# Performance work log

Measured on AMD Instinct MI355X. Metric: run time of the kernel, lower is better.

The kernel has to match this reference:

```python
import jax, jax.numpy as jnp
import numpy as np


def conv1x1(x, w, b):
    # x: [B,C,H,W], w: [O,C], b: [O]
    return jnp.einsum('bchw,oc->bohw', x, w) + b[None, :, None, None]


def dwconv(x, w):
    # depthwise conv, x: [B,C,H,W], w: [C,1,k,k], SAME padding (k odd, pad=k//2)
    return jax.lax.conv_general_dilated(
        x, w, window_strides=(1, 1), padding='SAME',
        dimension_numbers=('NCHW', 'OIHW', 'NCHW'),
        feature_group_count=x.shape[1])


def setup_inputs() -> dict:
    key = jax.random.key(0)
    ks = jax.random.split(key, 14)
    B, C, H, W = 16, 256, 64, 64
    OC = C // 16  # scale=16 -> 16
    WSCALE = 0.05
    r = lambda k, shape: jax.random.normal(k, shape, dtype=jnp.float32) * WSCALE
    return {
        'x': jax.random.normal(ks[0], (B, C, H, W), dtype=jnp.float32),
        'conv_w': r(ks[1], (C + 4, C)),           # 1x1 conv -> ctx (C) + gates (3+1)
        'conv_b': r(ks[2], (C + 4,)),
        'fw3': r(ks[3], (C, 1, 3, 3)),            # depthwise focal kernels
        'fw5': r(ks[4], (C, 1, 5, 5)),
        'fw7': r(ks[5], (C, 1, 7, 7)),
        'key_w': r(ks[6], (1, C)),                # Conv_key 1x1
        'key_b': r(ks[7], (1,)),
        'v1_w': r(ks[8], (OC, C)),                # Conv_value first 1x1
        'v1_b': r(ks[9], (OC,)),
        'ln_w': jnp.ones((OC,), dtype=jnp.float32),
        'ln_b': jnp.zeros((OC,), dtype=jnp.float32),
        'v2_w': r(ks[10], (C, OC)),               # Conv_value second 1x1
        'v2_b': r(ks[11], (C,)),
    }


def reference(x, conv_w, conv_b, fw3, fw5, fw7, key_w, key_b,
              v1_w, v1_b, ln_w, ln_b, v2_w, v2_b):
    B, C, H, W = x.shape
    # _contextAggregation
    t = conv1x1(x, conv_w, conv_b)          # [B, C+4, H, W]
    ctx, gates = t[:, :C], t[:, C:]         # [B,C,H,W], [B,4,H,W]
    ctx_all = jnp.zeros_like(ctx)
    for l, fw in enumerate((fw3, fw5, fw7)):
        ctx = jax.nn.gelu(dwconv(ctx, fw), approximate=False)  # torch GELU = exact erf
        ctx_all = ctx_all + ctx * gates[:, l:l + 1]
    ctx_global = jnp.mean(ctx, axis=(2, 3), keepdims=True)     # AdaptiveAvgPool2d(1)
    ctx_all = ctx_all + ctx_global * gates[:, 3:4]
    # GC-style channel attention: softmax over spatial positions
    k = conv1x1(ctx_all, key_w, key_b).reshape(B, H * W)       # [B, HW]
    k = jax.nn.softmax(k, axis=1)
    q = ctx_all.reshape(B, C, H * W)
    qk = jnp.einsum('bcn,bn->bc', q, k)[:, :, None, None]      # [B,C,1,1]
    # Conv_value: 1x1 -> LayerNorm([OC,1,1]) -> ReLU -> 1x1
    v = conv1x1(qk, v1_w, v1_b)                                # [B,OC,1,1]
    mu = jnp.mean(v, axis=(1, 2, 3), keepdims=True)
    var = jnp.var(v, axis=(1, 2, 3), keepdims=True)
    v = (v - mu) * jax.lax.rsqrt(var + 1e-5)
    v = v * ln_w[None, :, None, None] + ln_b[None, :, None, None]
    v = jax.nn.relu(v)
    v = conv1x1(v, v2_w, v2_b)                                 # [B,C,1,1]
    return ctx_all + v
```

## Files before the change

kernel.cpp:

```cpp
#include <hip/hip_runtime.h>

#define DEVFN __device__ __forceinline__

constexpr int B  = 16;
constexpr int C  = 256;
constexpr int N  = 64 * 64;
constexpr int O1 = C + 4;

typedef __attribute__((ext_vector_type(8)))  short bf16x8;
typedef __attribute__((ext_vector_type(4)))  short bf16x4;
typedef __attribute__((ext_vector_type(16))) float f32x16;
typedef __attribute__((ext_vector_type(2)))  _Float16 h2;
typedef unsigned short ushort_t;
typedef unsigned int   uint32;

DEVFN short f2bf(float f){
  union { float f; unsigned u; } p; p.f = f;
  unsigned r = p.u + 0x7fffu + ((p.u >> 16) & 1u);
  return (short)(r >> 16);
}
DEVFN unsigned pack2(float lo, float hi){
  return (unsigned)(ushort_t)f2bf(lo) | ((unsigned)(ushort_t)f2bf(hi) << 16);
}
DEVFN float lo2f(unsigned u){ union{unsigned u; float f;} p; p.u = u << 16; return p.f; }
DEVFN float hi2f(unsigned u){ union{unsigned u; float f;} p; p.u = u & 0xffff0000u; return p.f; }
DEVFN float bf2f(ushort_t s){ union{unsigned u; float f;} p; p.u = (unsigned)s << 16; return p.f; }

DEVFN float gelu_fast(float x){
  float s = x * x;
  float t = x * fmaf(s, 0.1029432f, 2.3022082f);
  float e = __builtin_amdgcn_exp2f(-t);
  return x * __builtin_amdgcn_rcpf(1.0f + e);
}

DEVFN float fdot2f(uint32 a, uint32 b, float c){
#if __has_builtin(__builtin_amdgcn_fdot2)
  return __builtin_amdgcn_fdot2(__builtin_bit_cast(h2, a),
                                __builtin_bit_cast(h2, b), c, false);
#else
  h2 ha = __builtin_bit_cast(h2, a), hb = __builtin_bit_cast(h2, b);
  return fmaf((float)ha.x, (float)hb.x, fmaf((float)ha.y, (float)hb.y, c));
#endif
}

DEVFN uint32 pkh(float a, float b){
  _Float16 ha = (_Float16)a, hb = (_Float16)b;
  return (uint32)__builtin_bit_cast(ushort_t, ha) |
         ((uint32)__builtin_bit_cast(ushort_t, hb) << 16);
}

__global__ __launch_bounds__(256)
void k_wbf(const float* __restrict__ w, ushort_t* __restrict__ wbf,
           const float* __restrict__ fw3, const float* __restrict__ fw5,
           const float* __restrict__ fw7, uint32* __restrict__ w3p,
           uint32* __restrict__ w5p, uint32* __restrict__ w7p,
           const float* __restrict__ x, ushort_t* __restrict__ xbf){
  if(blockIdx.x >= 321){
    const int blk = blockIdx.x - 321;
    const int b  = blk >> 5;
    const int kg = blk & 31;
    const float* xs = x + ((size_t)(b * 256 + kg * 8)) * N;
    ushort_t* xd = xbf + ((size_t)(b * 32 + kg)) * N * 8;
    #pragma unroll
    for(int it = 0; it < 4; it++){
      const int n = (it * 256 + threadIdx.x) * 4;
      float4 cv[8];
      #pragma unroll
      for(int j = 0; j < 8; j++) cv[j] = *(const float4*)(xs + (size_t)j * N + n);
      #pragma unroll
      for(int p = 0; p < 4; p++){
        uint4 v;
        v.x = pack2(((const float*)&cv[0])[p], ((const float*)&cv[1])[p]);
        v.y = pack2(((const float*)&cv[2])[p], ((const float*)&cv[3])[p]);
        v.z = pack2(((const float*)&cv[4])[p], ((const float*)&cv[5])[p]);
        v.w = pack2(((const float*)&cv[6])[p], ((const float*)&cv[7])[p]);
        *(uint4*)(xd + (size_t)(n + p) * 8) = v;
      }
    }
    return;
  }
  if(blockIdx.x == 320){
    const int c = threadIdx.x;
    #pragma unroll
    for(int ky = 0; ky < 3; ky++){
      const float* wr = fw3 + c * 9 + ky * 3;
      w3p[c * 6 + ky * 2 + 0] = pkh(wr[0], wr[1]);
      w3p[c * 6 + ky * 2 + 1] = pkh(wr[2], 0.f);
    }
    #pragma unroll
    for(int ky = 0; ky < 5; ky++){
      const float* wr = fw5 + c * 25 + ky * 5;
      w5p[c * 15 + ky * 3 + 0] = pkh(wr[0], wr[1]);
      w5p[c * 15 + ky * 3 + 1] = pkh(wr[2], wr[3]);
      w5p[c * 15 + ky * 3 + 2] = pkh(wr[4], 0.f);
    }
    #pragma unroll
    for(int ky = 0; ky < 7; ky++){
      const float* wr = fw7 + c * 49 + ky * 7;
      w7p[c * 28 + ky * 4 + 0] = pkh(wr[0], wr[1]);
      w7p[c * 28 + ky * 4 + 1] = pkh(wr[2], wr[3]);
      w7p[c * 28 + ky * 4 + 2] = pkh(wr[4], wr[5]);
      w7p[c * 28 + ky * 4 + 3] = pkh(wr[6], 0.f);
    }
    return;
  }
  int idx = blockIdx.x * 256 + threadIdx.x;
  int o = idx >> 8, cc = idx & 255;
  wbf[idx] = (o < O1) ? (ushort_t)f2bf(w[o * 256 + cc]) : (ushort_t)0;
}

__global__ __launch_bounds__(512, 6)
void k_conv1_mfma(const ushort_t* __restrict__ xbf, const ushort_t* __restrict__ wbf,
                  const float* __restrict__ conv_w, const float* __restrict__ bias,
                  ushort_t* __restrict__ ctxb, float* __restrict__ gates){
  __shared__ __align__(16) short wlds[2][4 * 256 * 8];
  __shared__ __align__(16) short xlds[2][4 * 64 * 8];
  __shared__ float sgw[4 * 256];
  __shared__ float sbias[256];
  const int tid  = threadIdx.x;
  const int wave = tid >> 6;
  const int lane = tid & 63;
  const int l31  = lane & 31;
  const int lhi  = lane >> 5;
  const int pg   = blockIdx.x;
  const int b    = pg >> 6;
  const int n0   = (pg & 63) * 64;

  #pragma unroll
  for(int i = 0; i < 2; i++) sgw[i * 512 + tid] = conv_w[256 * 256 + i * 512 + tid];
  if(tid < 256) sbias[tid] = bias[tid];
  const int gidx = tid >> 6;
  const int gn   = tid & 63;
  float gbias = (tid < 256) ? bias[256 + gidx] : 0.f;
  float gacc = 0.f;

  f32x16 acc[2];
  #pragma unroll
  for(int t = 0; t < 2; t++)
    #pragma unroll
    for(int r = 0; r < 16; r++) acc[t][r] = 0.f;

  auto glX = [&](int kc, int bf){
    if(tid < 256){
      const int kg = tid >> 6, n = tid & 63;
      const ushort_t* src = xbf + ((size_t)(b * 32 + (kc >> 3) + kg) * N + n0 + n) * 8;
      __builtin_amdgcn_global_load_lds(
          (const __attribute__((address_space(1))) unsigned int*)src,
          (__attribute__((address_space(3))) unsigned int*)&xlds[bf][(size_t)tid * 8],
          16, 0, 0);
    }
  };
  auto glW = [&](int kc, int bf){
    #pragma unroll
    for(int q = 0; q < 2; q++){
      const int pidx = q * 512 + tid;
      const int kg = pidx >> 8;
      const int m  = pidx & 255;
      const ushort_t* src = wbf + (size_t)m * 256 + kc + kg * 8;
      __builtin_amdgcn_global_load_lds(
          (const __attribute__((address_space(1))) unsigned int*)src,
          (__attribute__((address_space(3))) unsigned int*)&wlds[bf][(size_t)pidx * 8],
          16, 0, 0);
    }
  };
  auto mfmaC = [&](int bf){
    #pragma unroll
    for(int ks = 0; ks < 2; ks++){
      const int kg = ks * 2 + lhi;
      bf16x8 af = *(const bf16x8*)&wlds[bf][(kg * 256 + wave * 32 + l31) * 8];
      bf16x8 b0 = *(const bf16x8*)&xlds[bf][(kg * 64 + l31) * 8];
      bf16x8 b1 = *(const bf16x8*)&xlds[bf][(kg * 64 + 32 + l31) * 8];
      acc[0] = __builtin_amdgcn_mfma_f32_32x32x16_bf16(af, b0, acc[0], 0, 0, 0);
      acc[1] = __builtin_amdgcn_mfma_f32_32x32x16_bf16(af, b1, acc[1], 0, 0, 0);
    }
  };
  auto gateC = [&](int bf, int kc){
    if(tid < 256){
      float a = gacc;
      #pragma unroll
      for(int kg = 0; kg < 4; kg++){
        bf16x8 xv = *(const bf16x8*)&xlds[bf][(kg * 64 + gn) * 8];
        const float* gw = &sgw[gidx * 256 + kc + kg * 8];
        #pragma unroll
        for(int j = 0; j < 4; j++){
          unsigned u = ((const unsigned*)&xv)[j];
          a = fmaf(lo2f(u), gw[2 * j], a);
          a = fmaf(hi2f(u), gw[2 * j + 1], a);
        }
      }
      gacc = a;
    }
  };

  glX(0, 0); glW(0, 0);
  __syncthreads();
  #pragma unroll
  for(int c = 0; c < 7; c++){
    const int bf = c & 1;
    glX((c + 1) * 32, bf ^ 1);
    glW((c + 1) * 32, bf ^ 1);
    mfmaC(bf);
    gateC(bf, c * 32);
    __syncthreads();
  }
  mfmaC(1);
  gateC(1, 224);

  #pragma unroll
  for(int nt = 0; nt < 2; nt++){
    const int n = n0 + nt * 32 + l31;
    #pragma unroll
    for(int r = 0; r < 16; r++){
      const int row = (r & 3) + 8 * (r >> 2) + 4 * lhi;
      const int o = wave * 32 + row;
      const float v = acc[nt][r] + sbias[o];
      _Float16 hv = (_Float16)v;
      ctxb[((size_t)(b * 256 + o)) * N + n] = __builtin_bit_cast(ushort_t, hv);
    }
  }
  if(tid < 256)
    gates[((size_t)(b * 4 + gidx)) * N + n0 + gn] = gacc + gbias;
}

constexpr int SSTR = 72;

template<int K>
DEVFN void dw_stage_dot(const short* src, const uint32* __restrict__ wp,
                        int h, int w0, float* val){
  constexpr int R = K / 2;
  constexpr int PAIRS = (K + 2) / 2;
  float acc[8];
  #pragma unroll
  for(int i = 0; i < 8; i++) acc[i] = 0.f;
  #pragma unroll
  for(int ky = 0; ky < K; ky++){
    uint32 wk[PAIRS];
    #pragma unroll
    for(int t = 0; t < PAIRS; t++) wk[t] = wp[ky * PAIRS + t];
    const int r = h + ky - R;
    if((unsigned)r < 64u){
      const short* rp = &src[r * SSTR + w0];
      uint4 a0 = *(const uint4*)rp;
      uint4 a1 = *(const uint4*)(rp + 8);
      uint32 P[8] = {a0.x, a0.y, a0.z, a0.w, a1.x, a1.y, a1.z, a1.w};
      uint32 S[7];
      #pragma unroll
      for(int j = 0; j < 7; j++)
        S[j] = __builtin_amdgcn_alignbit(P[j + 1], P[j], 16);
      #pragma unroll
      for(int i = 0; i < 8; i++){
        int j0, useP;
        if      (K == 7){ useP =  (i & 1); j0 = (i + 1) >> 1; }
        else if (K == 5){ useP = !(i & 1); j0 = (i >> 1) + 1; }
        else            { useP =  (i & 1); j0 = (i >> 1) + ((i & 1) ? 2 : 1); }
        #pragma unroll
        for(int t = 0; t < PAIRS; t++){
          const uint32 a = useP ? P[j0 + t] : S[j0 + t];
          acc[i] = fdot2f(a, wk[t], acc[i]);
        }
      }
    }
  }
  #pragma unroll
  for(int i = 0; i < 8; i++) val[i] = gelu_fast(acc[i]);
}

DEVFN void store_row_h(short* dst, int h, int w0, const float* val){
  uint32 o0 = __builtin_bit_cast(uint32, __builtin_amdgcn_cvt_pkrtz(val[0], val[1]));
  uint32 o1 = __builtin_bit_cast(uint32, __builtin_amdgcn_cvt_pkrtz(val[2], val[3]));
  uint32 o2 = __builtin_bit_cast(uint32, __builtin_amdgcn_cvt_pkrtz(val[4], val[5]));
  uint32 o3 = __builtin_bit_cast(uint32, __builtin_amdgcn_cvt_pkrtz(val[6], val[7]));
  uint2 t0; t0.x = o0; t0.y = o1;
  uint2 t1; t1.x = o2; t1.y = o3;
  *(uint2*)&dst[h * SSTR + w0 + 4] = t0;
  *(uint2*)&dst[h * SSTR + w0 + 8] = t1;
}

__global__ __launch_bounds__(512, 8)
void k_dwchain(ushort_t* __restrict__ ctxb, const uint32* __restrict__ w3p,
               const uint32* __restrict__ w5p, const uint32* __restrict__ w7p,
               const float* __restrict__ gates){
  __shared__ __align__(16) short bufA[64 * SSTR];
  __shared__ __align__(16) short bufB[64 * SSTR];
  __shared__ float wred[8];
  const int tid = threadIdx.x;
  const int plane = blockIdx.x;
  const int b = plane >> 8;
  const int c = plane & 255;
  const int h  = tid >> 3;
  const int w0 = (tid & 7) * 8;
  const int nbase = h * 64 + w0;

  if(tid < 64){
    bf16x4 z = {0, 0, 0, 0};
    *(bf16x4*)&bufA[tid * SSTR] = z;  *(bf16x4*)&bufA[tid * SSTR + 68] = z;
    *(bf16x4*)&bufB[tid * SSTR] = z;  *(bf16x4*)&bufB[tid * SSTR + 68] = z;
  }
  {
    const uint4 iv = *(const uint4*)((const short*)ctxb + (size_t)plane * N + tid * 8);
    uint2 t0; t0.x = iv.x; t0.y = iv.y;
    uint2 t1; t1.x = iv.z; t1.y = iv.w;
    *(uint2*)&bufA[h * SSTR + w0 + 4] = t0;
    *(uint2*)&bufA[h * SSTR + w0 + 8] = t1;
  }
  __syncthreads();

  float ctxp[8];
  #pragma unroll
  for(int i = 0; i < 8; i++) ctxp[i] = 0.f;
  float val[8];

  dw_stage_dot<3>(bufA, w3p + c * 6, h, w0, val);
  {
    const float* gp = gates + ((size_t)(b * 4 + 0)) * N + nbase;
    float4 ga = *(const float4*)gp, gb = *(const float4*)(gp + 4);
    ctxp[0] = fmaf(val[0], ga.x, ctxp[0]); ctxp[1] = fmaf(val[1], ga.y, ctxp[1]);
    ctxp[2] = fmaf(val[2], ga.z, ctxp[2]); ctxp[3] = fmaf(val[3], ga.w, ctxp[3]);
    ctxp[4] = fmaf(val[4], gb.x, ctxp[4]); ctxp[5] = fmaf(val[5], gb.y, ctxp[5]);
    ctxp[6] = fmaf(val[6], gb.z, ctxp[6]); ctxp[7] = fmaf(val[7], gb.w, ctxp[7]);
    store_row_h(bufB, h, w0, val);
  }
  __syncthreads();

  dw_stage_dot<5>(bufB, w5p + c * 15, h, w0, val);
  {
    const float* gp = gates + ((size_t)(b * 4 + 1)) * N + nbase;
    float4 ga = *(const float4*)gp, gb = *(const float4*)(gp + 4);
    ctxp[0] = fmaf(val[0], ga.x, ctxp[0]); ctxp[1] = fmaf(val[1], ga.y, ctxp[1]);
    ctxp[2] = fmaf(val[2], ga.z, ctxp[2]); ctxp[3] = fmaf(val[3], ga.w, ctxp[3]);
    ctxp[4] = fmaf(val[4], gb.x, ctxp[4]); ctxp[5] = fmaf(val[5], gb.y, ctxp[5]);
    ctxp[6] = fmaf(val[6], gb.z, ctxp[6]); ctxp[7] = fmaf(val[7], gb.w, ctxp[7]);
    store_row_h(bufA, h, w0, val);
  }
  __syncthreads();

  dw_stage_dot<7>(bufA, w7p + c * 28, h, w0, val);
  float lsum = 0.f;
  {
    const float* gp = gates + ((size_t)(b * 4 + 2)) * N + nbase;
    float4 ga = *(const float4*)gp, gb = *(const float4*)(gp + 4);
    ctxp[0] = fmaf(val[0], ga.x, ctxp[0]); ctxp[1] = fmaf(val[1], ga.y, ctxp[1]);
    ctxp[2] = fmaf(val[2], ga.z, ctxp[2]); ctxp[3] = fmaf(val[3], ga.w, ctxp[3]);
    ctxp[4] = fmaf(val[4], gb.x, ctxp[4]); ctxp[5] = fmaf(val[5], gb.y, ctxp[5]);
    ctxp[6] = fmaf(val[6], gb.z, ctxp[6]); ctxp[7] = fmaf(val[7], gb.w, ctxp[7]);
    #pragma unroll
    for(int i = 0; i < 8; i++) lsum += val[i];
  }
  #pragma unroll
  for(int off = 32; off > 0; off >>= 1) lsum += __shfl_xor(lsum, off, 64);
  if((tid & 63) == 0) wred[tid >> 6] = lsum;
  __syncthreads();
  float mean = 0.f;
  #pragma unroll
  for(int i = 0; i < 8; i++) mean += wred[i];
  mean *= (1.0f / 4096.0f);

  {
    const float* gp = gates + ((size_t)(b * 4 + 3)) * N + nbase;
    float4 ga = *(const float4*)gp, gb = *(const float4*)(gp + 4);
    bf16x8 ov;
    ov[0] = f2bf(fmaf(mean, ga.x, ctxp[0])); ov[1] = f2bf(fmaf(mean, ga.y, ctxp[1]));
    ov[2] = f2bf(fmaf(mean, ga.z, ctxp[2])); ov[3] = f2bf(fmaf(mean, ga.w, ctxp[3]));
    ov[4] = f2bf(fmaf(mean, gb.x, ctxp[4])); ov[5] = f2bf(fmaf(mean, gb.y, ctxp[5]));
    ov[6] = f2bf(fmaf(mean, gb.z, ctxp[6])); ov[7] = f2bf(fmaf(mean, gb.w, ctxp[7]));
    *(bf16x8*)((short*)ctxb + (size_t)plane * N + nbase) = ov;
  }
}

__global__ __launch_bounds__(256)
void k_logits(const ushort_t* __restrict__ P, const float* __restrict__ key_w,
              const float* __restrict__ key_b, float* __restrict__ logits){
  __shared__ float kw[256];
  __shared__ float part[512];
  int tid = threadIdx.x;
  kw[tid] = key_w[tid];
  __syncthreads();
  int b  = blockIdx.x >> 5;
  int n0 = (blockIdx.x & 31) * 128;
  int cpart = tid >> 6, pxp = tid & 63;
  const ushort_t* pp = P + ((size_t)(b * 256 + cpart * 64)) * N + n0 + pxp * 2;
  float a0 = 0.f, a1 = 0.f;
  #pragma unroll 8
  for(int c = 0; c < 64; c++){
    unsigned u = *(const unsigned*)(pp + (size_t)c * N);
    float kwv = kw[cpart * 64 + c];
    a0 = fmaf(lo2f(u), kwv, a0);
    a1 = fmaf(hi2f(u), kwv, a1);
  }
  part[cpart * 128 + pxp * 2]     = a0;
  part[cpart * 128 + pxp * 2 + 1] = a1;
  __syncthreads();
  if(tid < 128){
    float l = part[tid] + part[128 + tid] + part[256 + tid] + part[384 + tid];
    logits[b * N + n0 + tid] = l + key_b[0];
  }
}

__global__ __launch_bounds__(256)
void k_qk(const ushort_t* __restrict__ P, const float* __restrict__ logits,
          float* __restrict__ qk){
  __shared__ float red[256];
  __shared__ float wred[4];
  const int plane = blockIdx.x, tid = threadIdx.x;
  const int b = plane >> 8;
  const int wave = tid >> 6, lane = tid & 63;
  const float2* lp = (const float2*)(logits + b * N);
  float2 l2[8];
  float m = -1e30f;
  #pragma unroll
  for(int i = 0; i < 8; i++){
    l2[i] = lp[tid + i * 256];
    m = fmaxf(m, fmaxf(l2[i].x, l2[i].y));
  }
  #pragma unroll
  for(int off = 32; off > 0; off >>= 1) m = fmaxf(m, __shfl_xor(m, off, 64));
  if(lane == 0) wred[wave] = m;
  __syncthreads();
  m = fmaxf(fmaxf(wred[0], wred[1]), fmaxf(wred[2], wred[3]));
  __syncthreads();
  float s = 0.f;
  #pragma unroll
  for(int i = 0; i < 8; i++){
    l2[i].x = __expf(l2[i].x - m);
    l2[i].y = __expf(l2[i].y - m);
    s += l2[i].x + l2[i].y;
  }
  #pragma unroll
  for(int off = 32; off > 0; off >>= 1) s += __shfl_xor(s, off, 64);
  if(lane == 0) wred[wave] = s;
  __syncthreads();
  const float stot = wred[0] + wred[1] + wred[2] + wred[3];
  const unsigned* pp = (const unsigned*)(P + (size_t)plane * N);
  float acc = 0.f;
  #pragma unroll
  for(int i = 0; i < 8; i++){
    unsigned u = pp[tid + i * 256];
    acc = fmaf(lo2f(u), l2[i].x, acc);
    acc = fmaf(hi2f(u), l2[i].y, acc);
  }
  red[tid] = acc; __syncthreads();
  for(int t = 128; t > 0; t >>= 1){
    if(tid < t) red[tid] += red[tid + t];
    __syncthreads();
  }
  if(tid == 0) qk[plane] = red[0] / stot;
}

__global__ __launch_bounds__(256)
void k_final(float* __restrict__ out, const ushort_t* __restrict__ ctxb,
             const float* __restrict__ qkb, const float* __restrict__ v1w,
             const float* __restrict__ v1b, const float* __restrict__ lnw,
             const float* __restrict__ lnb, const float* __restrict__ v2w,
             const float* __restrict__ v2b){
  __shared__ float part[256];
  __shared__ float v1s[16];
  __shared__ float bc[1];
  const int tid  = threadIdx.x;
  const int idx8 = blockIdx.x * 256 + tid;
  const int plane = idx8 >> 9;
  const int b = plane >> 8, c = plane & 255;
  const int oc = tid >> 4, ln = tid & 15;
  const float* qs = qkb + b * 256;
  float p = 0.f;
  #pragma unroll
  for(int j = 0; j < 16; j++){
    const int cc = ln + j * 16;
    p = fmaf(v1w[oc * 256 + cc], qs[cc], p);
  }
  part[tid] = p;
  __syncthreads();
  if(tid < 16){
    float s = v1b[tid];
    #pragma unroll
    for(int j = 0; j < 16; j++) s += part[tid * 16 + j];
    v1s[tid] = s;
  }
  __syncthreads();
  if(tid == 0){
    float mu = 0.f;
    #pragma unroll
    for(int i = 0; i < 16; i++) mu += v1s[i];
    mu *= (1.f / 16.f);
    float var = 0.f;
    #pragma unroll
    for(int i = 0; i < 16; i++){ float d = v1s[i] - mu; var += d * d; }
    var *= (1.f / 16.f);
    const float rs = rsqrtf(var + 1e-5f);
    float o = v2b[c];
    #pragma unroll
    for(int i = 0; i < 16; i++){
      float vv = (v1s[i] - mu) * rs * lnw[i] + lnb[i];
      o = fmaf(v2w[c * 16 + i], fmaxf(vv, 0.f), o);
    }
    bc[0] = o;
  }
  __syncthreads();
  const float vv = bc[0];
  const int off = (idx8 & 511) * 8;
  bf16x8 v = *(const bf16x8*)((const short*)ctxb + (size_t)plane * N + off);
  float4 o0, o1;
  o0.x = bf2f((ushort_t)v[0]) + vv; o0.y = bf2f((ushort_t)v[1]) + vv;
  o0.z = bf2f((ushort_t)v[2]) + vv; o0.w = bf2f((ushort_t)v[3]) + vv;
  o1.x = bf2f((ushort_t)v[4]) + vv; o1.y = bf2f((ushort_t)v[5]) + vv;
  o1.z = bf2f((ushort_t)v[6]) + vv; o1.w = bf2f((ushort_t)v[7]) + vv;
  float* op = out + (size_t)plane * N + off;
  *(float4*)op = o0;
  *(float4*)(op + 4) = o1;
}

extern "C" void kernel_launch(void* const* d_in, const int* in_sizes, int n_in,
                              void* d_out, int out_size, void* d_ws, size_t ws_size,
                              hipStream_t stream){
  const float* x      = (const float*)d_in[0];
  const float* conv_w = (const float*)d_in[1];
  const float* conv_b = (const float*)d_in[2];
  const float* fw3    = (const float*)d_in[3];
  const float* fw5    = (const float*)d_in[4];
  const float* fw7    = (const float*)d_in[5];
  const float* key_w  = (const float*)d_in[6];
  const float* key_b  = (const float*)d_in[7];
  const float* v1_w   = (const float*)d_in[8];
  const float* v1_b   = (const float*)d_in[9];
  const float* ln_w   = (const float*)d_in[10];
  const float* ln_b   = (const float*)d_in[11];
  const float* v2_w   = (const float*)d_in[12];
  const float* v2_b   = (const float*)d_in[13];
  float* out = (float*)d_out;

  const size_t PL = (size_t)B * C * N;
  char* p = (char*)d_ws;
  ushort_t* ctxb = (ushort_t*)p;  p += PL * sizeof(ushort_t);
  float* gates   = (float*)p;     p += (size_t)B * 4 * N * sizeof(float);
  float* kbuf    = (float*)p;     p += (size_t)B * N * sizeof(float);
  float* qkb     = (float*)p;     p += (size_t)B * C * sizeof(float);
  ushort_t* wbf  = (ushort_t*)p;  p += (size_t)320 * 256 * sizeof(ushort_t);
  uint32* w3p    = (uint32*)p;    p += (size_t)256 * 6 * sizeof(uint32);
  uint32* w5p    = (uint32*)p;    p += (size_t)256 * 15 * sizeof(uint32);
  uint32* w7p    = (uint32*)p;
  ushort_t* xbf  = (ushort_t*)d_out;

  k_wbf<<<833, 256, 0, stream>>>(conv_w, wbf, fw3, fw5, fw7, w3p, w5p, w7p,
                                 x, xbf);
  k_conv1_mfma<<<1024, 512, 0, stream>>>(xbf, wbf, conv_w, conv_b, ctxb, gates);
  k_dwchain<<<B * C, 512, 0, stream>>>(ctxb, w3p, w5p, w7p, gates);
  k_logits<<<512, 256, 0, stream>>>(ctxb, key_w, key_b, kbuf);
  k_qk<<<B * C, 256, 0, stream>>>(ctxb, kbuf, qkb);
  k_final<<<8192, 256, 0, stream>>>(out, ctxb, qkb, v1_w, v1_b, ln_w, ln_b,
                                    v2_w, v2_b);
}
```

Before: 260.3 us.

## Fuse fp32-to-bf16 input conversion into the 1x1 conv MFMA kernel

Drops the separate pass that converted x to an interleaved bf16 buffer in the output scratch. The conv kernel now loads fp32 x tiles directly into LDS and repacks them to bf16 in LDS. The weight tile becomes single-buffered and is loaded after a second barrier. This removes a full read and write of the intermediate bf16 tensor, at the cost of more LDS traffic, extra barriers per K step, and less overlap for the weight loads.

Measured after the change: 250.1 us. 1.04x faster.

```diff
diff --git a/kernel.cpp b/kernel.cpp
--- a/kernel.cpp
+++ b/kernel.cpp
@@ -53,32 +53,7 @@
 void k_wbf(const float* __restrict__ w, ushort_t* __restrict__ wbf,
            const float* __restrict__ fw3, const float* __restrict__ fw5,
            const float* __restrict__ fw7, uint32* __restrict__ w3p,
-           uint32* __restrict__ w5p, uint32* __restrict__ w7p,
-           const float* __restrict__ x, ushort_t* __restrict__ xbf){
-  if(blockIdx.x >= 321){
-    const int blk = blockIdx.x - 321;
-    const int b  = blk >> 5;
-    const int kg = blk & 31;
-    const float* xs = x + ((size_t)(b * 256 + kg * 8)) * N;
-    ushort_t* xd = xbf + ((size_t)(b * 32 + kg)) * N * 8;
-    #pragma unroll
-    for(int it = 0; it < 4; it++){
-      const int n = (it * 256 + threadIdx.x) * 4;
-      float4 cv[8];
-      #pragma unroll
-      for(int j = 0; j < 8; j++) cv[j] = *(const float4*)(xs + (size_t)j * N + n);
-      #pragma unroll
-      for(int p = 0; p < 4; p++){
-        uint4 v;
-        v.x = pack2(((const float*)&cv[0])[p], ((const float*)&cv[1])[p]);
-        v.y = pack2(((const float*)&cv[2])[p], ((const float*)&cv[3])[p]);
-        v.z = pack2(((const float*)&cv[4])[p], ((const float*)&cv[5])[p]);
-        v.w = pack2(((const float*)&cv[6])[p], ((const float*)&cv[7])[p]);
-        *(uint4*)(xd + (size_t)(n + p) * 8) = v;
-      }
-    }
-    return;
-  }
+           uint32* __restrict__ w5p, uint32* __restrict__ w7p){
   if(blockIdx.x == 320){
     const int c = threadIdx.x;
     #pragma unroll
@@ -110,10 +85,11 @@
 }
 
 __global__ __launch_bounds__(512, 6)
-void k_conv1_mfma(const ushort_t* __restrict__ xbf, const ushort_t* __restrict__ wbf,
+void k_conv1_mfma(const float* __restrict__ x, const ushort_t* __restrict__ wbf,
                   const float* __restrict__ conv_w, const float* __restrict__ bias,
                   ushort_t* __restrict__ ctxb, float* __restrict__ gates){
-  __shared__ __align__(16) short wlds[2][4 * 256 * 8];
+  __shared__ __align__(16) short wlds[4 * 256 * 8];
+  __shared__ __align__(16) float xf32[2][32 * 64];
   __shared__ __align__(16) short xlds[2][4 * 64 * 8];
   __shared__ float sgw[4 * 256];
   __shared__ float sbias[256];
@@ -126,31 +102,17 @@
   const int b    = pg >> 6;
   const int n0   = (pg & 63) * 64;
 
-  #pragma unroll
-  for(int i = 0; i < 2; i++) sgw[i * 512 + tid] = conv_w[256 * 256 + i * 512 + tid];
-  if(tid < 256) sbias[tid] = bias[tid];
-  const int gidx = tid >> 6;
-  const int gn   = tid & 63;
-  float gbias = (tid < 256) ? bias[256 + gidx] : 0.f;
-  float gacc = 0.f;
-
-  f32x16 acc[2];
-  #pragma unroll
-  for(int t = 0; t < 2; t++)
-    #pragma unroll
-    for(int r = 0; r < 16; r++) acc[t][r] = 0.f;
-
-  auto glX = [&](int kc, int bf){
-    if(tid < 256){
-      const int kg = tid >> 6, n = tid & 63;
-      const ushort_t* src = xbf + ((size_t)(b * 32 + (kc >> 3) + kg) * N + n0 + n) * 8;
-      __builtin_amdgcn_global_load_lds(
-          (const __attribute__((address_space(1))) unsigned int*)src,
-          (__attribute__((address_space(3))) unsigned int*)&xlds[bf][(size_t)tid * 8],
-          16, 0, 0);
-    }
+  const float* xpb = x + (size_t)b * C * N + n0;
+
+  auto glXf32 = [&](int kc, int bf){
+    const int kg = tid >> 4, nq = tid & 15;
+    const float* src = xpb + (size_t)(kc + kg) * N + nq * 4;
+    __builtin_amdgcn_global_load_lds(
+        (const __attribute__((address_space(1))) unsigned int*)src,
+        (__attribute__((address_space(3))) unsigned int*)&xf32[bf][(size_t)tid * 4],
+        16, 0, 0);
   };
-  auto glW = [&](int kc, int bf){
+  auto glW = [&](int kc){
     #pragma unroll
     for(int q = 0; q < 2; q++){
       const int pidx = q * 512 + tid;
@@ -159,21 +121,45 @@
       const ushort_t* src = wbf + (size_t)m * 256 + kc + kg * 8;
       __builtin_amdgcn_global_load_lds(
           (const __attribute__((address_space(1))) unsigned int*)src,
-          (__attribute__((address_space(3))) unsigned int*)&wlds[bf][(size_t)pidx * 8],
+          (__attribute__((address_space(3))) unsigned int*)&wlds[(size_t)pidx * 8],
           16, 0, 0);
     }
   };
-  auto mfmaC = [&](int bf){
+  auto repack = [&](int bf){
+    const int half = tid & 1, n = (tid >> 1) & 63, kgrp = tid >> 7;
+    const float* s = &xf32[bf][(kgrp * 8 + half * 4) * 64 + n];
+    bf16x4 v;
+    v[0] = f2bf(s[0]);   v[1] = f2bf(s[64]);
+    v[2] = f2bf(s[128]); v[3] = f2bf(s[192]);
+    *(bf16x4*)&xlds[bf][(kgrp * 64 + n) * 8 + half * 4] = v;
+  };
+  auto mfmaC = [&](int bf, f32x16* acc){
     #pragma unroll
     for(int ks = 0; ks < 2; ks++){
       const int kg = ks * 2 + lhi;
-      bf16x8 af = *(const bf16x8*)&wlds[bf][(kg * 256 + wave * 32 + l31) * 8];
+      bf16x8 af = *(const bf16x8*)&wlds[(kg * 256 + wave * 32 + l31) * 8];
       bf16x8 b0 = *(const bf16x8*)&xlds[bf][(kg * 64 + l31) * 8];
       bf16x8 b1 = *(const bf16x8*)&xlds[bf][(kg * 64 + 32 + l31) * 8];
       acc[0] = __builtin_amdgcn_mfma_f32_32x32x16_bf16(af, b0, acc[0], 0, 0, 0);
       acc[1] = __builtin_amdgcn_mfma_f32_32x32x16_bf16(af, b1, acc[1], 0, 0, 0);
     }
   };
+
+  glXf32(0, 0); glW(0);
+  #pragma unroll
+  for(int i = 0; i < 2; i++) sgw[i * 512 + tid] = conv_w[256 * 256 + i * 512 + tid];
+  if(tid < 256) sbias[tid] = bias[tid];
+  const int gidx = tid >> 6;
+  const int gn   = tid & 63;
+  float gbias = (tid < 256) ? bias[256 + gidx] : 0.f;
+  float gacc = 0.f;
+
+  f32x16 acc[2];
+  #pragma unroll
+  for(int t = 0; t < 2; t++)
+    #pragma unroll
+    for(int r = 0; r < 16; r++) acc[t][r] = 0.f;
+
   auto gateC = [&](int bf, int kc){
     if(tid < 256){
       float a = gacc;
@@ -192,18 +178,21 @@
     }
   };
 
-  glX(0, 0); glW(0, 0);
+  __syncthreads();
+  repack(0);
   __syncthreads();
   #pragma unroll
   for(int c = 0; c < 7; c++){
     const int bf = c & 1;
-    glX((c + 1) * 32, bf ^ 1);
-    glW((c + 1) * 32, bf ^ 1);
-    mfmaC(bf);
+    glXf32((c + 1) * 32, bf ^ 1);
+    mfmaC(bf, acc);
     gateC(bf, c * 32);
     __syncthreads();
-  }
-  mfmaC(1);
+    glW((c + 1) * 32);
+    repack(bf ^ 1);
+    __syncthreads();
+  }
+  mfmaC(1, acc);
   gateC(1, 224);
 
   #pragma unroll
@@ -537,11 +526,9 @@
   uint32* w3p    = (uint32*)p;    p += (size_t)256 * 6 * sizeof(uint32);
   uint32* w5p    = (uint32*)p;    p += (size_t)256 * 15 * sizeof(uint32);
   uint32* w7p    = (uint32*)p;
-  ushort_t* xbf  = (ushort_t*)d_out;
-
-  k_wbf<<<833, 256, 0, stream>>>(conv_w, wbf, fw3, fw5, fw7, w3p, w5p, w7p,
-                                 x, xbf);
-  k_conv1_mfma<<<1024, 512, 0, stream>>>(xbf, wbf, conv_w, conv_b, ctxb, gates);
+
+  k_wbf<<<321, 256, 0, stream>>>(conv_w, wbf, fw3, fw5, fw7, w3p, w5p, w7p);
+  k_conv1_mfma<<<1024, 512, 0, stream>>>(x, wbf, conv_w, conv_b, ctxb, gates);
   k_dwchain<<<B * C, 512, 0, stream>>>(ctxb, w3p, w5p, w7p, gates);
   k_logits<<<512, 256, 0, stream>>>(ctxb, key_w, key_b, kbuf);
   k_qk<<<B * C, 256, 0, stream>>>(ctxb, kbuf, qkb);
```
